# Performance work log

Hardware: AMD Instinct MI355X
Metric: run time of the kernel (lower is better)

Reference implementation:

```python
import jax, jax.numpy as jnp
import numpy as np

H, DH = 8, 32            # heads, per-head dim
F_DIM = H * DH           # hidden_channels = 256
N_P, N_A = 100000, 50000 # paper / author node counts
E_AP, E_PA, E_PP = 300000, 300000, 500000
N_CLASSES = 32


def _seg_softmax(alpha, idx, n):
    # softmax over edges grouped by destination node (per head)
    m = jax.ops.segment_max(alpha, idx, num_segments=n)
    m = jnp.where(jnp.isfinite(m), m, 0.0)  # nodes with no in-edges
    e = jnp.exp(alpha - m[idx])
    s = jax.ops.segment_sum(e, idx, num_segments=n)
    return e / (s[idx] + 1e-16)


def _edge_attn(h_src, h_dst, a_src, a_dst, src, dst, n_dst):
    # h_*: [N, H, DH]; a_*: [H, DH]; src/dst: [E]
    als = jnp.einsum('nhd,hd->nh', h_src, a_src)
    ald = jnp.einsum('nhd,hd->nh', h_dst, a_dst)
    alpha = jax.nn.leaky_relu(als[src] + ald[dst], negative_slope=0.2)  # [E,H]
    a = _seg_softmax(alpha, dst, n_dst)
    out = jax.ops.segment_sum(h_src[src] * a[:, :, None], dst, num_segments=n_dst)
    return jax.nn.relu(out).reshape(n_dst, F_DIM)


def _semantic(xs, kW, kb, q):
    # semantic (edge-type level) attention, PyG HANConv 'group'
    X = jnp.stack(xs)  # [K, N, F]
    score = jnp.einsum('f,kf->k', q, jnp.tanh(X @ kW + kb).mean(axis=1))
    attn = jax.nn.softmax(score)
    return jnp.einsum('k,knf->nf', attn, X)


def _han_layer(xP, xA, prm, edg):
    (W_P, b_P, W_A, b_A, aS_AP, aD_AP, aS_PA, aD_PA, aS_PP, aD_PP, kW, kb, q) = prm
    sAP, dAP, sPA, dPA, sPP, dPP = edg
    hP = (xP @ W_P + b_P).reshape(-1, H, DH)
    hA = (xA @ W_A + b_A).reshape(-1, H, DH)
    oAP = _edge_attn(hA, hP, aS_AP, aD_AP, sAP, dAP, N_P)  # author->paper
    oPP = _edge_attn(hP, hP, aS_PP, aD_PP, sPP, dPP, N_P)  # paper->paper
    oPA = _edge_attn(hP, hA, aS_PA, aD_PA, sPA, dPA, N_A)  # paper->author
    newP = _semantic([oAP, oPP], kW, kb, q)
    newA = _semantic([oPA], kW, kb, q)
    return newP, newA


def setup_inputs() -> dict:
    ks = iter(jax.random.split(jax.random.key(0), 80))
    def nrm(shape, scale=1.0):
        return jax.random.normal(next(ks), shape, dtype=jnp.float32) * scale
    def idx(n, high):
        return jax.random.randint(next(ks), (n,), 0, high, dtype=jnp.int32)
    inp = {}
    inp['x_P'] = nrm((N_P, 512))
    inp['x_A'] = nrm((N_A, 256))
    inp['src_AP'] = idx(E_AP, N_A); inp['dst_AP'] = idx(E_AP, N_P)
    inp['src_PA'] = idx(E_PA, N_P); inp['dst_PA'] = idx(E_PA, N_A)
    inp['src_PP'] = idx(E_PP, N_P); inp['dst_PP'] = idx(E_PP, N_P)
    for l, inP, inA in ((0, 512, 256), (1, F_DIM, F_DIM)):
        inp[f'W{l}_P'] = nrm((inP, F_DIM), 0.05)
        inp[f'b{l}_P'] = jnp.zeros((F_DIM,), jnp.float32)
        inp[f'W{l}_A'] = nrm((inA, F_DIM), 0.05)
        inp[f'b{l}_A'] = jnp.zeros((F_DIM,), jnp.float32)
        for et in ('AP', 'PA', 'PP'):
            inp[f'as{l}_{et}'] = nrm((H, DH), 0.1)
            inp[f'ad{l}_{et}'] = nrm((H, DH), 0.1)
        inp[f'k{l}_W'] = nrm((F_DIM, F_DIM), 0.05)
        inp[f'k{l}_b'] = jnp.zeros((F_DIM,), jnp.float32)
        inp[f'q{l}'] = nrm((F_DIM,), 0.1)
    inp['lin_W'] = nrm((F_DIM, N_CLASSES), 0.05)
    inp['lin_b'] = jnp.zeros((N_CLASSES,), jnp.float32)
    return inp


def reference(x_P, x_A, src_AP, dst_AP, src_PA, dst_PA, src_PP, dst_PP,
              W0_P, b0_P, W0_A, b0_A, as0_AP, ad0_AP, as0_PA, ad0_PA, as0_PP, ad0_PP, k0_W, k0_b, q0,
              W1_P, b1_P, W1_A, b1_A, as1_AP, ad1_AP, as1_PA, ad1_PA, as1_PP, ad1_PP, k1_W, k1_b, q1,
              lin_W, lin_b):
    edg = (src_AP, dst_AP, src_PA, dst_PA, src_PP, dst_PP)
    p0 = (W0_P, b0_P, W0_A, b0_A, as0_AP, ad0_AP, as0_PA, ad0_PA, as0_PP, ad0_PP, k0_W, k0_b, q0)
    p1 = (W1_P, b1_P, W1_A, b1_A, as1_AP, ad1_AP, as1_PA, ad1_PA, as1_PP, ad1_PP, k1_W, k1_b, q1)
    xP, xA = _han_layer(x_P, x_A, p0, edg)
    xP, xA = _han_layer(xP, xA, p1, edg)
    # final classifier on labeled_class = 'paper' (dropout is eval-mode no-op)
    return xP @ lin_W + lin_b
```

## Files before the change

kernel.cpp:

```cpp
#include <hip/hip_runtime.h>
#include <math.h>

typedef unsigned short u16;
typedef u16 ushort8 __attribute__((ext_vector_type(8)));
typedef __bf16 bf16x8 __attribute__((ext_vector_type(8)));
typedef float floatx4 __attribute__((ext_vector_type(4)));

__device__ __forceinline__ float bf2f(u16 u) {
  union { unsigned int i; float f; } v; v.i = ((unsigned int)u) << 16; return v.f;
}
__device__ __forceinline__ u16 f2bf(float f) {
  union { float f; unsigned int i; } v; v.f = f;
  return (u16)((v.i + 0x7fffu + ((v.i >> 16) & 1u)) >> 16);
}

#define CEILDIV(a, b) (((a) + (b) - 1) / (b))

typedef const __attribute__((address_space(1))) unsigned int ga_u32;
typedef __attribute__((address_space(3))) unsigned int lds_u32;
__device__ __forceinline__ void gload16(const u16* g, u16* l) {
  __builtin_amdgcn_global_load_lds((ga_u32*)g, (lds_u32*)l, 16, 0, 0);
}

__global__ void k_transpose(const float* __restrict__ W, u16* __restrict__ Wt, int K, int N) {
  int t = blockIdx.x * blockDim.x + threadIdx.x;
  if (t >= K * N) return;
  int n = t / K, k = t - n * K;
  Wt[t] = f2bf(W[k * N + n]);
}

__global__ void k_hist3(const int* __restrict__ d0, int E0, int* __restrict__ c0,
                        const int* __restrict__ d1, int E1, int* __restrict__ c1,
                        const int* __restrict__ d2, int E2, int* __restrict__ c2) {
  int t = blockIdx.x * blockDim.x + threadIdx.x;
  if (t < E0) atomicAdd(&c0[d0[t]], 1);
  else if (t < E0 + E1) atomicAdd(&c1[d1[t - E0]], 1);
  else if (t < E0 + E1 + E2) atomicAdd(&c2[d2[t - E0 - E1]], 1);
}

__global__ void k_scatter3(
    const int* __restrict__ d0, const int* __restrict__ s0v, int E0,
    const int* __restrict__ rp0, int* __restrict__ cur0, int* __restrict__ es0,
    const int* __restrict__ d1, const int* __restrict__ s1v, int E1,
    const int* __restrict__ rp1, int* __restrict__ cur1, int* __restrict__ es1,
    const int* __restrict__ d2, const int* __restrict__ s2v, int E2,
    const int* __restrict__ rp2, int* __restrict__ cur2, int* __restrict__ es2) {
  int t = blockIdx.x * blockDim.x + threadIdx.x;
  if (t < E0) {
    int d = d0[t];
    int p = atomicAdd(&cur0[d], 1);
    es0[rp0[d] + p] = s0v[t];
  } else if (t < E0 + E1) {
    int u = t - E0;
    int d = d1[u];
    int p = atomicAdd(&cur1[d], 1);
    es1[rp1[d] + p] = s1v[u];
  } else if (t < E0 + E1 + E2) {
    int u = t - E0 - E1;
    int d = d2[u];
    int p = atomicAdd(&cur2[d], 1);
    es2[rp2[d] + p] = s2v[u];
  }
}

__device__ __forceinline__ void seg_map(int b, int& seg, int& bs, int& n) {
  if (b < 98) { seg = 0; bs = b; n = 100000; }
  else if (b < 196) { seg = 1; bs = b - 98; n = 100000; }
  else { seg = 2; bs = b - 196; n = 50000; }
}

__global__ __launch_bounds__(256) void k_scan_a(
    const int* __restrict__ c0, const int* __restrict__ c1, const int* __restrict__ c2,
    int* __restrict__ bsum) {
  int seg, bs, n;
  seg_map(blockIdx.x, seg, bs, n);
  const int* cnt = seg == 0 ? c0 : (seg == 1 ? c1 : c2);
  int t = threadIdx.x;
  int base = bs * 1024 + t * 4;
  int s = 0;
#pragma unroll
  for (int j = 0; j < 4; j++) { int i = base + j; if (i < n) s += cnt[i]; }
#pragma unroll
  for (int o = 1; o < 64; o <<= 1) s += __shfl_xor(s, o);
  __shared__ int wt[4];
  int lane = t & 63, w = t >> 6;
  if (lane == 0) wt[w] = s;
  __syncthreads();
  if (t == 0) bsum[seg * 256 + bs] = wt[0] + wt[1] + wt[2] + wt[3];
}

__global__ __launch_bounds__(256) void k_scan_b(
    const int* __restrict__ bsum, int* __restrict__ bbase,
    int* __restrict__ rp0, int* __restrict__ rp1, int* __restrict__ rp2) {
  __shared__ int sm[256];
  int t = threadIdx.x;
  for (int seg = 0; seg < 3; ++seg) {
    int nb = (seg == 2) ? 49 : 98;
    int n = (seg == 2) ? 50000 : 100000;
    int v = (t < nb) ? bsum[seg * 256 + t] : 0;
    sm[t] = v;
    __syncthreads();
    for (int o = 1; o < 256; o <<= 1) {
      int u = (t >= o) ? sm[t - o] : 0;
      __syncthreads();
      sm[t] += u;
      __syncthreads();
    }
    if (t < nb) bbase[seg * 256 + t] = sm[t] - v;
    if (t == 255) {
      int* rp = seg == 0 ? rp0 : (seg == 1 ? rp1 : rp2);
      rp[n] = sm[255];
    }
    __syncthreads();
  }
}

__global__ __launch_bounds__(256) void k_scan_c(
    const int* __restrict__ c0, const int* __restrict__ c1, const int* __restrict__ c2,
    const int* __restrict__ bbase,
    int* __restrict__ rp0, int* __restrict__ rp1, int* __restrict__ rp2) {
  int seg, bs, n;
  seg_map(blockIdx.x, seg, bs, n);
  const int* cnt = seg == 0 ? c0 : (seg == 1 ? c1 : c2);
  int* rp = seg == 0 ? rp0 : (seg == 1 ? rp1 : rp2);
  int t = threadIdx.x;
  int base = bs * 1024 + t * 4;
  int c[4];
  int s = 0;
#pragma unroll
  for (int j = 0; j < 4; j++) { int i = base + j; c[j] = (i < n) ? cnt[i] : 0; s += c[j]; }
  int lane = t & 63, w = t >> 6;
  int incl = s;
#pragma unroll
  for (int o = 1; o < 64; o <<= 1) { int u = __shfl_up(incl, o); if (lane >= o) incl += u; }
  __shared__ int wt[4];
  if (lane == 63) wt[w] = incl;
  __syncthreads();
  int wb = 0;
#pragma unroll
  for (int j = 0; j < 4; j++) if (j < w) wb += wt[j];
  int thr = bbase[seg * 256 + bs] + wb + incl - s;
#pragma unroll
  for (int j = 0; j < 4; j++) { int i = base + j; if (i < n) rp[i] = thr; thr += c[j]; }
}

#define G3_BM 128
#define G3_BN 256
#define G3_BK 32

template <int SRC, int MODE>
__global__ __launch_bounds__(512, 4) void k_gemm3(
    const void* __restrict__ Av, const u16* __restrict__ A2, const float* __restrict__ attn,
    const u16* __restrict__ Bt, const float* __restrict__ bias,
    u16* __restrict__ Cb, float* __restrict__ colsum, int M, int K) {
  __shared__ __align__(16) u16 sm[2][(G3_BM + G3_BN) * G3_BK];
  int tid = threadIdx.x;
  int lane = tid & 63, wid = tid >> 6;
  int wm = wid >> 2, wn = wid & 3;
  int quad = lane >> 4, l16 = lane & 15;
  int m0 = blockIdx.x * G3_BM;

  float a0s = 0.f, a1s = 0.f;
  if (SRC == 1) { a0s = attn[0]; a1s = attn[1]; }

  int gr_ = tid >> 2;
  int gc_ = (tid & 3) * 8;
  int arow = m0 + gr_; if (arow >= M) arow = M - 1;
  const u16* gaB = (SRC != 2) ? (const u16*)Av + (size_t)arow * K + gc_ : nullptr;
  const u16* ga2 = (SRC == 1) ? A2 + (size_t)arow * K + gc_ : nullptr;
  const float* gaF = (SRC == 2) ? (const float*)Av + (size_t)arow * K + gc_ : nullptr;
  const u16* gb0 = Bt + (size_t)gr_ * K + gc_;
  const u16* gb1 = Bt + (size_t)(128 + gr_) * K + gc_;
  const int laA = wid * 512;
  const int laB0 = 4096 + wid * 512;
  const int laB1 = 8192 + wid * 512;

  floatx4 acc[4][4];
#pragma unroll
  for (int i = 0; i < 4; i++)
#pragma unroll
    for (int j = 0; j < 4; j++) acc[i][j] = (floatx4){0.f, 0.f, 0.f, 0.f};

  auto stage = [&](int buf, int k0) {
    u16* sa = sm[buf];
    if (SRC == 0) {
      gload16(gaB + k0, sa + laA);
    } else if (SRC == 2) {
      const floatx4* p = (const floatx4*)(gaF + k0);
      floatx4 v0 = p[0], v1 = p[1];
      u16 t[8];
#pragma unroll
      for (int j = 0; j < 4; j++) { t[j] = f2bf(v0[j]); t[4 + j] = f2bf(v1[j]); }
      *(ushort8*)(sa + laA + (lane << 3)) = *(ushort8*)t;
    } else {
      ushort8 u = *(const ushort8*)(gaB + k0);
      ushort8 w = *(const ushort8*)(ga2 + k0);
      u16 t[8];
#pragma unroll
      for (int j = 0; j < 8; j++) t[j] = f2bf(a0s * bf2f(u[j]) + a1s * bf2f(w[j]));
      *(ushort8*)(sa + laA + (lane << 3)) = *(ushort8*)t;
    }
    gload16(gb0 + k0, sa + laB0);
    gload16(gb1 + k0, sa + laB1);
  };

  stage(0, 0);
  __syncthreads();

  int nk = K / G3_BK;
  for (int t = 0; t < nk; ++t) {
    int cur = t & 1;
    if (t + 1 < nk) stage(cur ^ 1, (t + 1) * G3_BK);
    const u16* Ab = sm[cur];
    const u16* Bb = sm[cur] + G3_BM * G3_BK;
    bf16x8 af[4], bfr[4];
#pragma unroll
    for (int mi = 0; mi < 4; mi++)
      af[mi] = *(const bf16x8*)(Ab + (wm * 64 + mi * 16 + l16) * G3_BK + quad * 8);
#pragma unroll
    for (int ni = 0; ni < 4; ni++)
      bfr[ni] = *(const bf16x8*)(Bb + (wn * 64 + ni * 16 + l16) * G3_BK + quad * 8);
#pragma unroll
    for (int mi = 0; mi < 4; mi++)
#pragma unroll
      for (int ni = 0; ni < 4; ni++)
        acc[mi][ni] = __builtin_amdgcn_mfma_f32_16x16x32_bf16(af[mi], bfr[ni], acc[mi][ni], 0, 0, 0);
    __syncthreads();
  }

  if (MODE == 1) {
#pragma unroll
    for (int ni = 0; ni < 4; ni++) {
      int gc = wn * 64 + ni * 16 + l16;
      float bv = bias[gc];
      float part = 0.f;
#pragma unroll
      for (int mi = 0; mi < 4; mi++) {
#pragma unroll
        for (int r = 0; r < 4; r++) {
          int gr = m0 + wm * 64 + mi * 16 + quad * 4 + r;
          if (gr < M) {
            float v = acc[mi][ni][r] + bv;
            float e2 = __expf(2.f * v);
            part += 1.f - 2.f / (e2 + 1.f);
          }
        }
      }
      part += __shfl_xor(part, 16);
      part += __shfl_xor(part, 32);
      if (lane < 16) atomicAdd(&colsum[gc], part);
    }
  } else {
    float* smf = (float*)sm;
    float* tw = smf + wid * 16 * 68;
#pragma unroll
    for (int mi = 0; mi < 4; mi++) {
#pragma unroll
      for (int ni = 0; ni < 4; ni++)
#pragma unroll
        for (int r = 0; r < 4; r++)
          tw[(quad * 4 + r) * 68 + ni * 16 + l16] = acc[mi][ni][r];
      int row = lane >> 2, cq = (lane & 3) * 16;
      int gr = m0 + wm * 64 + mi * 16 + row;
      if (gr < M) {
        int gc0 = wn * 64 + cq;
        u16 ob[16];
#pragma unroll
        for (int j = 0; j < 16; j++) ob[j] = f2bf(tw[row * 68 + cq + j] + bias[gc0 + j]);
        *(ushort8*)(Cb + (size_t)gr * 256 + gc0) = *(ushort8*)ob;
        *(ushort8*)(Cb + (size_t)gr * 256 + gc0 + 8) = *(ushort8*)(ob + 8);
      }
    }
  }
}

#define BM 128
#define BN 128
#define BK 32

__global__ __launch_bounds__(256) void k_gemm2_cls(
    const u16* __restrict__ A, const u16* __restrict__ A2, const float* __restrict__ attn,
    const u16* __restrict__ Bt, const float* __restrict__ bias,
    float* __restrict__ Cf, int M, int N, int K) {
  __shared__ __align__(16) u16 sm[2][2][BM * BK];
  int tid = threadIdx.x;
  int lane = tid & 63, wid = tid >> 6;
  int wm = wid >> 1, wn = wid & 1;
  int quad = lane >> 4, l16 = lane & 15;
  int m0 = blockIdx.x * BM, n0 = 0;

  float a0s = attn[0], a1s = attn[1];

  int sr = lane >> 2;
  int sc = (lane & 3) * 8;
  int ra0 = m0 + wid * 32 + sr;
  int ra1 = ra0 + 16;
  int rb0 = n0 + wid * 32 + sr;
  int rb1 = rb0 + 16;
  if (ra0 >= M) ra0 = M - 1;
  if (ra1 >= M) ra1 = M - 1;
  if (rb0 >= N) rb0 = N - 1;
  if (rb1 >= N) rb1 = N - 1;
  const u16* ga0 = A + (size_t)ra0 * K + sc;
  const u16* ga1 = A + (size_t)ra1 * K + sc;
  const u16* g2a0 = A2 + (size_t)ra0 * K + sc;
  const u16* g2a1 = A2 + (size_t)ra1 * K + sc;
  const u16* gb0 = Bt + (size_t)rb0 * K + sc;
  const u16* gb1 = Bt + (size_t)rb1 * K + sc;
  const int la = wid * 32 * BK;
  const int lb = la + 16 * BK;

  floatx4 acc[4][4];
#pragma unroll
  for (int i = 0; i < 4; i++)
#pragma unroll
    for (int j = 0; j < 4; j++) acc[i][j] = (floatx4){0.f, 0.f, 0.f, 0.f};

  auto stage = [&](int buf, int k0) {
    u16* sa = &sm[buf][0][0];
    u16* sb = &sm[buf][1][0];
    ushort8 u0 = *(const ushort8*)(ga0 + k0);
    ushort8 w0 = *(const ushort8*)(g2a0 + k0);
    ushort8 u1 = *(const ushort8*)(ga1 + k0);
    ushort8 w1 = *(const ushort8*)(g2a1 + k0);
    u16 t0[8], t1[8];
#pragma unroll
    for (int j = 0; j < 8; j++) {
      t0[j] = f2bf(a0s * bf2f(u0[j]) + a1s * bf2f(w0[j]));
      t1[j] = f2bf(a0s * bf2f(u1[j]) + a1s * bf2f(w1[j]));
    }
    *(ushort8*)(sa + la + lane * 8) = *(ushort8*)t0;
    *(ushort8*)(sa + lb + lane * 8) = *(ushort8*)t1;
    gload16(gb0 + k0, sb + la);
    gload16(gb1 + k0, sb + lb);
  };

  stage(0, 0);
  __syncthreads();

  int nk = K / BK;
  for (int t = 0; t < nk; ++t) {
    int cur = t & 1;
    if (t + 1 < nk) stage(cur ^ 1, (t + 1) * BK);
    const u16* Ab = &sm[cur][0][0];
    const u16* Bb = &sm[cur][1][0];
    bf16x8 af[4], bfr[4];
#pragma unroll
    for (int mi = 0; mi < 4; mi++)
      af[mi] = *(const bf16x8*)(Ab + (wm * 64 + mi * 16 + l16) * BK + quad * 8);
#pragma unroll
    for (int ni = 0; ni < 4; ni++)
      bfr[ni] = *(const bf16x8*)(Bb + (wn * 64 + ni * 16 + l16) * BK + quad * 8);
#pragma unroll
    for (int mi = 0; mi < 4; mi++)
#pragma unroll
      for (int ni = 0; ni < 4; ni++)
        acc[mi][ni] = __builtin_amdgcn_mfma_f32_16x16x32_bf16(af[mi], bfr[ni], acc[mi][ni], 0, 0, 0);
    __syncthreads();
  }

#pragma unroll
  for (int ni = 0; ni < 4; ni++) {
    int gc = n0 + wn * 64 + ni * 16 + l16;
    if (gc >= N) continue;
    float bv = bias[gc];
#pragma unroll
    for (int mi = 0; mi < 4; mi++) {
#pragma unroll
      for (int r = 0; r < 4; r++) {
        int gr = m0 + wm * 64 + mi * 16 + quad * 4 + r;
        if (gr < M) Cf[(size_t)gr * N + gc] = acc[mi][ni][r] + bv;
      }
    }
  }
}

__global__ void k_logits(const u16* __restrict__ h, int N,
                         const float* __restrict__ a0, const float* __restrict__ a1,
                         const float* __restrict__ a2, const float* __restrict__ a3,
                         float* __restrict__ o0, float* __restrict__ o1,
                         float* __restrict__ o2, float* __restrict__ o3) {
  int t = blockIdx.x * blockDim.x + threadIdx.x;
  int n = t >> 3, hh = t & 7;
  if (n >= N) return;
  const ushort8* hp = (const ushort8*)(h + (size_t)n * 256 + hh * 32);
  float d0 = 0.f, d1 = 0.f, d2 = 0.f, d3 = 0.f;
#pragma unroll
  for (int q = 0; q < 4; q++) {
    ushort8 v = hp[q];
#pragma unroll
    for (int j = 0; j < 8; j++) {
      float f = bf2f(v[j]);
      int idx = hh * 32 + q * 8 + j;
      d0 += f * a0[idx];
      d1 += f * a1[idx];
      if (a2) d2 += f * a2[idx];
      if (a3) d3 += f * a3[idx];
    }
  }
  o0[t] = d0;
  o1[t] = d1;
  if (o2) o2[t] = d2;
  if (o3) o3[t] = d3;
}

__global__ __launch_bounds__(256) void k_attn_agg(
    const int* __restrict__ rp, const int* __restrict__ esrc,
    const float* __restrict__ als, const float* __restrict__ ald,
    const u16* __restrict__ hsrc, u16* __restrict__ out, int Ndst) {
  int wid = threadIdx.x >> 6, lane = threadIdx.x & 63;
  int n = blockIdx.x * 4 + wid;
  if (n >= Ndst) return;
  int hh = lane >> 3;
  int b = rp[n], e = rp[n + 1];
  float av = ald[n * 8 + hh];
  float m = -1e30f, s = 0.f;
  float a0 = 0.f, a1 = 0.f, a2 = 0.f, a3 = 0.f;
  int i = b;
  for (; i + 3 < e; i += 4) {
    int s0 = esrc[i], s1 = esrc[i + 1], s2 = esrc[i + 2], s3 = esrc[i + 3];
    float x0 = als[s0 * 8 + hh] + av, x1 = als[s1 * 8 + hh] + av;
    float x2 = als[s2 * 8 + hh] + av, x3 = als[s3 * 8 + hh] + av;
    ushort4 v0 = *(const ushort4*)(hsrc + (size_t)s0 * 256 + lane * 4);
    ushort4 v1 = *(const ushort4*)(hsrc + (size_t)s1 * 256 + lane * 4);
    ushort4 v2 = *(const ushort4*)(hsrc + (size_t)s2 * 256 + lane * 4);
    ushort4 v3 = *(const ushort4*)(hsrc + (size_t)s3 * 256 + lane * 4);
    x0 = x0 > 0.f ? x0 : 0.2f * x0;
    x1 = x1 > 0.f ? x1 : 0.2f * x1;
    x2 = x2 > 0.f ? x2 : 0.2f * x2;
    x3 = x3 > 0.f ? x3 : 0.2f * x3;
    float mx = fmaxf(fmaxf(x0, x1), fmaxf(x2, x3));
    if (mx > m) {
      float r = __expf(m - mx);
      s *= r; a0 *= r; a1 *= r; a2 *= r; a3 *= r;
      m = mx;
    }
    float w0 = __expf(x0 - m), w1 = __expf(x1 - m);
    float w2 = __expf(x2 - m), w3 = __expf(x3 - m);
    s += (w0 + w1) + (w2 + w3);
    a0 += w0 * bf2f(v0.x) + w1 * bf2f(v1.x) + w2 * bf2f(v2.x) + w3 * bf2f(v3.x);
    a1 += w0 * bf2f(v0.y) + w1 * bf2f(v1.y) + w2 * bf2f(v2.y) + w3 * bf2f(v3.y);
    a2 += w0 * bf2f(v0.z) + w1 * bf2f(v1.z) + w2 * bf2f(v2.z) + w3 * bf2f(v3.z);
    a3 += w0 * bf2f(v0.w) + w1 * bf2f(v1.w) + w2 * bf2f(v2.w) + w3 * bf2f(v3.w);
  }
  for (; i < e; ++i) {
    int s0 = esrc[i];
    float x0 = als[s0 * 8 + hh] + av;
    ushort4 v0 = *(const ushort4*)(hsrc + (size_t)s0 * 256 + lane * 4);
    x0 = x0 > 0.f ? x0 : 0.2f * x0;
    if (x0 > m) {
      float r = __expf(m - x0);
      s *= r; a0 *= r; a1 *= r; a2 *= r; a3 *= r;
      m = x0;
    }
    float w0 = __expf(x0 - m);
    s += w0;
    a0 += w0 * bf2f(v0.x);
    a1 += w0 * bf2f(v0.y);
    a2 += w0 * bf2f(v0.z);
    a3 += w0 * bf2f(v0.w);
  }
  float inv = 1.f / (s + 1e-16f);
  a0 *= inv; a1 *= inv; a2 *= inv; a3 *= inv;
  ushort4 o;
  o.x = f2bf(a0 > 0.f ? a0 : 0.f);
  o.y = f2bf(a1 > 0.f ? a1 : 0.f);
  o.z = f2bf(a2 > 0.f ? a2 : 0.f);
  o.w = f2bf(a3 > 0.f ? a3 : 0.f);
  *(ushort4*)(out + (size_t)n * 256 + lane * 4) = o;
}

__global__ void k_scores(const float* __restrict__ cs0, const float* __restrict__ cs1,
                         const float* __restrict__ q, float invN, float* __restrict__ attn) {
  int lane = threadIdx.x;
  float p0 = 0.f, p1 = 0.f;
  for (int f = lane; f < 256; f += 64) {
    float qv = q[f];
    p0 += qv * cs0[f];
    p1 += qv * cs1[f];
  }
  for (int o = 32; o > 0; o >>= 1) {
    p0 += __shfl_down(p0, o);
    p1 += __shfl_down(p1, o);
  }
  if (lane == 0) {
    float s0 = p0 * invN, s1 = p1 * invN;
    float mx = fmaxf(s0, s1);
    float e0 = __expf(s0 - mx), e1 = __expf(s1 - mx);
    float den = e0 + e1;
    attn[0] = e0 / den;
    attn[1] = e1 / den;
  }
}

extern "C" void kernel_launch(void* const* d_in, const int* in_sizes, int n_in,
                              void* d_out, int out_size, void* d_ws, size_t ws_size,
                              hipStream_t stream) {
  const int NP = 100000, NA = 50000;
  const int EAP = 300000, EPA = 300000, EPP = 500000;

  const float* xP = (const float*)d_in[0];
  const float* xA = (const float*)d_in[1];
  const int* srcAP = (const int*)d_in[2];
  const int* dstAP = (const int*)d_in[3];
  const int* srcPA = (const int*)d_in[4];
  const int* dstPA = (const int*)d_in[5];
  const int* srcPP = (const int*)d_in[6];
  const int* dstPP = (const int*)d_in[7];
  const float *W_P[2], *b_P[2], *W_A[2], *b_A[2];
  const float *asAP[2], *adAP[2], *asPA[2], *adPA[2], *asPP[2], *adPP[2];
  const float *kW[2], *kb[2], *qv[2];
  for (int l = 0; l < 2; ++l) {
    int base = 8 + l * 13;
    W_P[l] = (const float*)d_in[base + 0];
    b_P[l] = (const float*)d_in[base + 1];
    W_A[l] = (const float*)d_in[base + 2];
    b_A[l] = (const float*)d_in[base + 3];
    asAP[l] = (const float*)d_in[base + 4];
    adAP[l] = (const float*)d_in[base + 5];
    asPA[l] = (const float*)d_in[base + 6];
    adPA[l] = (const float*)d_in[base + 7];
    asPP[l] = (const float*)d_in[base + 8];
    adPP[l] = (const float*)d_in[base + 9];
    kW[l] = (const float*)d_in[base + 10];
    kb[l] = (const float*)d_in[base + 11];
    qv[l] = (const float*)d_in[base + 12];
  }
  const float* linW = (const float*)d_in[34];
  const float* linb = (const float*)d_in[35];

  char* ws = (char*)d_ws;
  size_t off = 0;
  auto alloc = [&](size_t bytes) -> char* {
    char* p = ws + off;
    off += (bytes + 255) & ~(size_t)255;
    return p;
  };
  u16* P1 = (u16*)alloc((size_t)NP * 256 * 2);
  u16* P2 = (u16*)alloc((size_t)NP * 256 * 2);
  u16* A1 = (u16*)alloc((size_t)NA * 256 * 2);
  u16* A2 = (u16*)alloc((size_t)NA * 256 * 2);
  u16* P3 = (u16*)alloc((size_t)NP * 256 * 2);
  float* ldAP_P = (float*)alloc((size_t)NP * 8 * 4);
  float* lsPA_P = (float*)alloc((size_t)NP * 8 * 4);
  float* lsPP_P = (float*)alloc((size_t)NP * 8 * 4);
  float* ldPP_P = (float*)alloc((size_t)NP * 8 * 4);
  float* lsAP_A = (float*)alloc((size_t)NA * 8 * 4);
  float* ldPA_A = (float*)alloc((size_t)NA * 8 * 4);
  u16* wtP0 = (u16*)alloc(256 * 512 * 2);
  u16* wtA0 = (u16*)alloc(256 * 256 * 2);
  u16* wtP1 = (u16*)alloc(256 * 256 * 2);
  u16* wtA1 = (u16*)alloc(256 * 256 * 2);
  u16* kwt0 = (u16*)alloc(256 * 256 * 2);
  u16* kwt1 = (u16*)alloc(256 * 256 * 2);
  u16* lwt = (u16*)alloc(32 * 256 * 2);
  int* rpAP = (int*)alloc((NP + 1) * 4);
  int* rpPP = (int*)alloc((NP + 1) * 4);
  int* rpPA = (int*)alloc((NA + 1) * 4);
  int* eiAP = (int*)alloc((size_t)EAP * 4);
  int* eiPP = (int*)alloc((size_t)EPP * 4);
  int* eiPA = (int*)alloc((size_t)EPA * 4);
  int* bsum = (int*)alloc(768 * 4);
  int* bbase = (int*)alloc(768 * 4);
  size_t zbytes = (size_t)(4 * NP + 2 * NA) * 4 + 4 * 256 * 4;
  char* zblock = alloc(zbytes);
  int* cntAP = (int*)zblock;
  int* cntPP = cntAP + NP;
  int* cntPA = cntPP + NP;
  int* curAP = cntPA + NA;
  int* curPP = curAP + NP;
  int* curPA = curPP + NP;
  float* cs = (float*)(curPA + NA);
  float* attnBuf = (float*)alloc(256);

  u16* HP = A1;
  u16* hA0 = P2;
  u16* P2b = P2 + (size_t)NA * 256;

  (void)hipMemsetAsync((void*)zblock, 0, zbytes, stream);

  k_transpose<<<CEILDIV(512 * 256, 256), 256, 0, stream>>>(W_P[0], wtP0, 512, 256);
  k_transpose<<<CEILDIV(256 * 256, 256), 256, 0, stream>>>(W_A[0], wtA0, 256, 256);
  k_transpose<<<CEILDIV(256 * 256, 256), 256, 0, stream>>>(W_P[1], wtP1, 256, 256);
  k_transpose<<<CEILDIV(256 * 256, 256), 256, 0, stream>>>(W_A[1], wtA1, 256, 256);
  k_transpose<<<CEILDIV(256 * 256, 256), 256, 0, stream>>>(kW[0], kwt0, 256, 256);
  k_transpose<<<CEILDIV(256 * 256, 256), 256, 0, stream>>>(kW[1], kwt1, 256, 256);
  k_transpose<<<CEILDIV(256 * 32, 256), 256, 0, stream>>>(linW, lwt, 256, 32);

  k_hist3<<<CEILDIV(EAP + EPP + EPA, 256), 256, 0, stream>>>(
      dstAP, EAP, cntAP, dstPP, EPP, cntPP, dstPA, EPA, cntPA);
  k_scan_a<<<245, 256, 0, stream>>>(cntAP, cntPP, cntPA, bsum);
  k_scan_b<<<1, 256, 0, stream>>>(bsum, bbase, rpAP, rpPP, rpPA);
  k_scan_c<<<245, 256, 0, stream>>>(cntAP, cntPP, cntPA, bbase, rpAP, rpPP, rpPA);
  k_scatter3<<<CEILDIV(EAP + EPP + EPA, 256), 256, 0, stream>>>(
      dstAP, srcAP, EAP, rpAP, curAP, eiAP,
      dstPP, srcPP, EPP, rpPP, curPP, eiPP,
      dstPA, srcPA, EPA, rpPA, curPA, eiPA);

  int gP = CEILDIV(NP, G3_BM), gA = CEILDIV(NA, G3_BM);

  k_gemm3<2, 0><<<gP, 512, 0, stream>>>(xP, nullptr, nullptr, wtP0, b_P[0], HP, nullptr, NP, 512);
  k_gemm3<2, 0><<<gA, 512, 0, stream>>>(xA, nullptr, nullptr, wtA0, b_A[0], hA0, nullptr, NA, 256);

  k_logits<<<CEILDIV(NP * 8, 256), 256, 0, stream>>>(
      HP, NP, adAP[0], asPA[0], asPP[0], adPP[0], ldAP_P, lsPA_P, lsPP_P, ldPP_P);
  k_logits<<<CEILDIV(NA * 8, 256), 256, 0, stream>>>(
      hA0, NA, asAP[0], adPA[0], nullptr, nullptr, lsAP_A, ldPA_A, nullptr, nullptr);
  k_attn_agg<<<CEILDIV(NP, 4), 256, 0, stream>>>(rpPP, eiPP, lsPP_P, ldPP_P, HP, P1, NP);
  k_attn_agg<<<CEILDIV(NA, 4), 256, 0, stream>>>(rpPA, eiPA, lsPA_P, ldPA_A, HP, P2b, NA);
  k_attn_agg<<<CEILDIV(NP, 4), 256, 0, stream>>>(rpAP, eiAP, lsAP_A, ldAP_P, hA0, HP, NP);
  k_gemm3<0, 1><<<gP, 512, 0, stream>>>(HP, nullptr, nullptr, kwt0, kb[0], nullptr, cs, NP, 256);
  k_gemm3<0, 1><<<gP, 512, 0, stream>>>(P1, nullptr, nullptr, kwt0, kb[0], nullptr, cs + 256, NP, 256);
  k_scores<<<1, 64, 0, stream>>>(cs, cs + 256, qv[0], 1.0f / NP, attnBuf);
  k_gemm3<1, 0><<<gP, 512, 0, stream>>>(HP, P1, attnBuf, wtP1, b_P[1], P3, nullptr, NP, 256);

  k_gemm3<0, 0><<<gA, 512, 0, stream>>>(P2b, nullptr, nullptr, wtA1, b_A[1], hA0, nullptr, NA, 256);
  k_logits<<<CEILDIV(NP * 8, 256), 256, 0, stream>>>(
      P3, NP, adAP[1], asPA[1], asPP[1], adPP[1], ldAP_P, lsPA_P, lsPP_P, ldPP_P);
  k_logits<<<CEILDIV(NA * 8, 256), 256, 0, stream>>>(
      hA0, NA, asAP[1], adPA[1], nullptr, nullptr, lsAP_A, ldPA_A, nullptr, nullptr);
  k_attn_agg<<<CEILDIV(NP, 4), 256, 0, stream>>>(rpPP, eiPP, lsPP_P, ldPP_P, P3, P1, NP);
  k_attn_agg<<<CEILDIV(NP, 4), 256, 0, stream>>>(rpAP, eiAP, lsAP_A, ldAP_P, hA0, HP, NP);
  k_gemm3<0, 1><<<gP, 512, 0, stream>>>(HP, nullptr, nullptr, kwt1, kb[1], nullptr, cs + 512, NP, 256);
  k_gemm3<0, 1><<<gP, 512, 0, stream>>>(P1, nullptr, nullptr, kwt1, kb[1], nullptr, cs + 768, NP, 256);
  k_scores<<<1, 64, 0, stream>>>(cs + 512, cs + 768, qv[1], 1.0f / NP, attnBuf + 2);

  k_gemm2_cls<<<CEILDIV(NP, BM), 256, 0, stream>>>(
      HP, P1, attnBuf + 2, lwt, linb, (float*)d_out, NP, 32, 256);
}
```

Measured before the change: 1.370 ms.

## Fuse attention logits into GEMM epilogue and batch small kernels into combined launches

Computes the per-head attention logits inside the projection GEMM epilogue, so the separate logits kernels no longer re-read the bf16 hidden features. The three (then two) edge-attention aggregation launches are merged into one multi-segment kernel, the paired colsum GEMMs become a single double-grid launch, and the seven weight transposes become one launch. Buffers are reassigned (P3/HP swapped) so the aggregated outputs do not overwrite inputs still needed. This cuts launch overhead and one full pass over the node features, at the cost of extra register pressure and FMA work in the GEMM epilogue, computed from fp32 values before bf16 rounding.

```diff
diff --git a/kernel.cpp b/kernel.cpp
--- a/kernel.cpp
+++ b/kernel.cpp
@@ -22,11 +22,26 @@
   __builtin_amdgcn_global_load_lds((ga_u32*)g, (lds_u32*)l, 16, 0, 0);
 }
 
-__global__ void k_transpose(const float* __restrict__ W, u16* __restrict__ Wt, int K, int N) {
+__global__ void k_transpose7(
+    const float* __restrict__ W0, u16* __restrict__ T0,
+    const float* __restrict__ W1, u16* __restrict__ T1,
+    const float* __restrict__ W2, u16* __restrict__ T2,
+    const float* __restrict__ W3, u16* __restrict__ T3,
+    const float* __restrict__ W4, u16* __restrict__ T4,
+    const float* __restrict__ W5, u16* __restrict__ T5,
+    const float* __restrict__ W6, u16* __restrict__ T6) {
   int t = blockIdx.x * blockDim.x + threadIdx.x;
-  if (t >= K * N) return;
-  int n = t / K, k = t - n * K;
-  Wt[t] = f2bf(W[k * N + n]);
+  const float* W; u16* T; int K, N, u;
+  if (t < 131072) { W = W0; T = T0; K = 512; N = 256; u = t; }
+  else if (t < 196608) { W = W1; T = T1; K = 256; N = 256; u = t - 131072; }
+  else if (t < 262144) { W = W2; T = T2; K = 256; N = 256; u = t - 196608; }
+  else if (t < 327680) { W = W3; T = T3; K = 256; N = 256; u = t - 262144; }
+  else if (t < 393216) { W = W4; T = T4; K = 256; N = 256; u = t - 327680; }
+  else if (t < 458752) { W = W5; T = T5; K = 256; N = 256; u = t - 393216; }
+  else if (t < 466944) { W = W6; T = T6; K = 256; N = 32; u = t - 458752; }
+  else return;
+  int n = u / K, k = u - n * K;
+  T[u] = f2bf(W[k * N + n]);
 }
 
 __global__ void k_hist3(const int* __restrict__ d0, int E0, int* __restrict__ c0,
@@ -148,17 +163,26 @@
 #define G3_BN 256
 #define G3_BK 32
 
-template <int SRC, int MODE>
+template <int SRC, int MODE, int NL, int PAIR>
 __global__ __launch_bounds__(512, 4) void k_gemm3(
     const void* __restrict__ Av, const u16* __restrict__ A2, const float* __restrict__ attn,
     const u16* __restrict__ Bt, const float* __restrict__ bias,
-    u16* __restrict__ Cb, float* __restrict__ colsum, int M, int K) {
+    u16* __restrict__ Cb, float* __restrict__ colsum, int M, int K,
+    const float* __restrict__ av0, const float* __restrict__ av1,
+    const float* __restrict__ av2, const float* __restrict__ av3,
+    float* __restrict__ lo0, float* __restrict__ lo1,
+    float* __restrict__ lo2, float* __restrict__ lo3) {
   __shared__ __align__(16) u16 sm[2][(G3_BM + G3_BN) * G3_BK];
+  int bid = blockIdx.x;
+  if (PAIR) {
+    int half = (int)gridDim.x >> 1;
+    if (bid >= half) { bid -= half; Av = (const void*)A2; colsum += 256; }
+  }
   int tid = threadIdx.x;
   int lane = tid & 63, wid = tid >> 6;
   int wm = wid >> 2, wn = wid & 3;
   int quad = lane >> 4, l16 = lane & 15;
-  int m0 = blockIdx.x * G3_BM;
+  int m0 = bid * G3_BM;
 
   float a0s = 0.f, a1s = 0.f;
   if (SRC == 1) { a0s = attn[0]; a1s = attn[1]; }
@@ -262,20 +286,40 @@
           tw[(quad * 4 + r) * 68 + ni * 16 + l16] = acc[mi][ni][r];
       int row = lane >> 2, cq = (lane & 3) * 16;
       int gr = m0 + wm * 64 + mi * 16 + row;
+      int gc0 = wn * 64 + cq;
+      u16 ob[16];
+      float p0 = 0.f, p1 = 0.f, p2 = 0.f, p3 = 0.f;
+#pragma unroll
+      for (int j = 0; j < 16; j++) {
+        float v = tw[row * 68 + cq + j] + bias[gc0 + j];
+        ob[j] = f2bf(v);
+        if (NL > 0) {
+          int col = gc0 + j;
+          p0 += v * av0[col];
+          p1 += v * av1[col];
+          if (NL > 2) { p2 += v * av2[col]; p3 += v * av3[col]; }
+        }
+      }
       if (gr < M) {
-        int gc0 = wn * 64 + cq;
-        u16 ob[16];
-#pragma unroll
-        for (int j = 0; j < 16; j++) ob[j] = f2bf(tw[row * 68 + cq + j] + bias[gc0 + j]);
         *(ushort8*)(Cb + (size_t)gr * 256 + gc0) = *(ushort8*)ob;
         *(ushort8*)(Cb + (size_t)gr * 256 + gc0 + 8) = *(ushort8*)(ob + 8);
       }
+      if (NL > 0) {
+        p0 += __shfl_xor(p0, 1);
+        p1 += __shfl_xor(p1, 1);
+        if (NL > 2) { p2 += __shfl_xor(p2, 1); p3 += __shfl_xor(p3, 1); }
+        if ((lane & 1) == 0 && gr < M) {
+          int hd = wn * 2 + ((lane & 3) >> 1);
+          lo0[gr * 8 + hd] = p0;
+          lo1[gr * 8 + hd] = p1;
+          if (NL > 2) { lo2[gr * 8 + hd] = p2; lo3[gr * 8 + hd] = p3; }
+        }
+      }
     }
   }
 }
 
 #define BM 128
-#define BN 128
 #define BK 32
 
 __global__ __launch_bounds__(256) void k_gemm2_cls(
@@ -375,41 +419,27 @@
   }
 }
 
-__global__ void k_logits(const u16* __restrict__ h, int N,
-                         const float* __restrict__ a0, const float* __restrict__ a1,
-                         const float* __restrict__ a2, const float* __restrict__ a3,
-                         float* __restrict__ o0, float* __restrict__ o1,
-                         float* __restrict__ o2, float* __restrict__ o3) {
-  int t = blockIdx.x * blockDim.x + threadIdx.x;
-  int n = t >> 3, hh = t & 7;
-  if (n >= N) return;
-  const ushort8* hp = (const ushort8*)(h + (size_t)n * 256 + hh * 32);
-  float d0 = 0.f, d1 = 0.f, d2 = 0.f, d3 = 0.f;
-#pragma unroll
-  for (int q = 0; q < 4; q++) {
-    ushort8 v = hp[q];
-#pragma unroll
-    for (int j = 0; j < 8; j++) {
-      float f = bf2f(v[j]);
-      int idx = hh * 32 + q * 8 + j;
-      d0 += f * a0[idx];
-      d1 += f * a1[idx];
-      if (a2) d2 += f * a2[idx];
-      if (a3) d3 += f * a3[idx];
-    }
-  }
-  o0[t] = d0;
-  o1[t] = d1;
-  if (o2) o2[t] = d2;
-  if (o3) o3[t] = d3;
-}
-
-__global__ __launch_bounds__(256) void k_attn_agg(
-    const int* __restrict__ rp, const int* __restrict__ esrc,
-    const float* __restrict__ als, const float* __restrict__ ald,
-    const u16* __restrict__ hsrc, u16* __restrict__ out, int Ndst) {
+__global__ __launch_bounds__(256) void k_attn3(
+    int nb0, int nb1,
+    const int* __restrict__ rp0, const int* __restrict__ es0, const float* __restrict__ als0,
+    const float* __restrict__ ald0, const u16* __restrict__ h0, u16* __restrict__ out0, int N0,
+    const int* __restrict__ rp1, const int* __restrict__ es1, const float* __restrict__ als1,
+    const float* __restrict__ ald1, const u16* __restrict__ h1, u16* __restrict__ out1, int N1,
+    const int* __restrict__ rp2, const int* __restrict__ es2, const float* __restrict__ als2,
+    const float* __restrict__ ald2, const u16* __restrict__ h2, u16* __restrict__ out2, int N2) {
+  int bid = blockIdx.x;
+  const int* rp; const int* esrc; const float* als; const float* ald;
+  const u16* hsrc; u16* out; int Ndst;
+  if (bid < nb0) { rp = rp0; esrc = es0; als = als0; ald = ald0; hsrc = h0; out = out0; Ndst = N0; }
+  else if (bid < nb0 + nb1) {
+    bid -= nb0;
+    rp = rp1; esrc = es1; als = als1; ald = ald1; hsrc = h1; out = out1; Ndst = N1;
+  } else {
+    bid -= nb0 + nb1;
+    rp = rp2; esrc = es2; als = als2; ald = ald2; hsrc = h2; out = out2; Ndst = N2;
+  }
   int wid = threadIdx.x >> 6, lane = threadIdx.x & 63;
-  int n = blockIdx.x * 4 + wid;
+  int n = bid * 4 + wid;
   if (n >= Ndst) return;
   int hh = lane >> 3;
   int b = rp[n], e = rp[n + 1];
@@ -579,13 +609,9 @@
 
   (void)hipMemsetAsync((void*)zblock, 0, zbytes, stream);
 
-  k_transpose<<<CEILDIV(512 * 256, 256), 256, 0, stream>>>(W_P[0], wtP0, 512, 256);
-  k_transpose<<<CEILDIV(256 * 256, 256), 256, 0, stream>>>(W_A[0], wtA0, 256, 256);
-  k_transpose<<<CEILDIV(256 * 256, 256), 256, 0, stream>>>(W_P[1], wtP1, 256, 256);
-  k_transpose<<<CEILDIV(256 * 256, 256), 256, 0, stream>>>(W_A[1], wtA1, 256, 256);
-  k_transpose<<<CEILDIV(256 * 256, 256), 256, 0, stream>>>(kW[0], kwt0, 256, 256);
-  k_transpose<<<CEILDIV(256 * 256, 256), 256, 0, stream>>>(kW[1], kwt1, 256, 256);
-  k_transpose<<<CEILDIV(256 * 32, 256), 256, 0, stream>>>(linW, lwt, 256, 32);
+  k_transpose7<<<CEILDIV(466944, 256), 256, 0, stream>>>(
+      W_P[0], wtP0, W_A[0], wtA0, W_P[1], wtP1, W_A[1], wtA1,
+      kW[0], kwt0, kW[1], kwt1, linW, lwt);
 
   k_hist3<<<CEILDIV(EAP + EPP + EPA, 256), 256, 0, stream>>>(
       dstAP, EAP, cntAP, dstPP, EPP, cntPP, dstPA, EPA, cntPA);
@@ -598,33 +624,45 @@
       dstPA, srcPA, EPA, rpPA, curPA, eiPA);
 
   int gP = CEILDIV(NP, G3_BM), gA = CEILDIV(NA, G3_BM);
-
-  k_gemm3<2, 0><<<gP, 512, 0, stream>>>(xP, nullptr, nullptr, wtP0, b_P[0], HP, nullptr, NP, 512);
-  k_gemm3<2, 0><<<gA, 512, 0, stream>>>(xA, nullptr, nullptr, wtA0, b_A[0], hA0, nullptr, NA, 256);
-
-  k_logits<<<CEILDIV(NP * 8, 256), 256, 0, stream>>>(
-      HP, NP, adAP[0], asPA[0], asPP[0], adPP[0], ldAP_P, lsPA_P, lsPP_P, ldPP_P);
-  k_logits<<<CEILDIV(NA * 8, 256), 256, 0, stream>>>(
-      hA0, NA, asAP[0], adPA[0], nullptr, nullptr, lsAP_A, ldPA_A, nullptr, nullptr);
-  k_attn_agg<<<CEILDIV(NP, 4), 256, 0, stream>>>(rpPP, eiPP, lsPP_P, ldPP_P, HP, P1, NP);
-  k_attn_agg<<<CEILDIV(NA, 4), 256, 0, stream>>>(rpPA, eiPA, lsPA_P, ldPA_A, HP, P2b, NA);
-  k_attn_agg<<<CEILDIV(NP, 4), 256, 0, stream>>>(rpAP, eiAP, lsAP_A, ldAP_P, hA0, HP, NP);
-  k_gemm3<0, 1><<<gP, 512, 0, stream>>>(HP, nullptr, nullptr, kwt0, kb[0], nullptr, cs, NP, 256);
-  k_gemm3<0, 1><<<gP, 512, 0, stream>>>(P1, nullptr, nullptr, kwt0, kb[0], nullptr, cs + 256, NP, 256);
+  int bP = CEILDIV(NP, 4), bA = CEILDIV(NA, 4);
+
+  k_gemm3<2, 0, 4, 0><<<gP, 512, 0, stream>>>(
+      xP, nullptr, nullptr, wtP0, b_P[0], HP, nullptr, NP, 512,
+      adAP[0], asPA[0], asPP[0], adPP[0], ldAP_P, lsPA_P, lsPP_P, ldPP_P);
+  k_gemm3<2, 0, 2, 0><<<gA, 512, 0, stream>>>(
+      xA, nullptr, nullptr, wtA0, b_A[0], hA0, nullptr, NA, 256,
+      asAP[0], adPA[0], nullptr, nullptr, lsAP_A, ldPA_A, nullptr, nullptr);
+
+  k_attn3<<<bP + bA + bP, 256, 0, stream>>>(
+      bP, bA,
+      rpPP, eiPP, lsPP_P, ldPP_P, HP, P1, NP,
+      rpPA, eiPA, lsPA_P, ldPA_A, HP, P2b, NA,
+      rpAP, eiAP, lsAP_A, ldAP_P, hA0, P3, NP);
+
+  k_gemm3<0, 1, 0, 1><<<2 * gP, 512, 0, stream>>>(
+      P3, P1, nullptr, kwt0, kb[0], nullptr, cs, NP, 256,
+      nullptr, nullptr, nullptr, nullptr, nullptr, nullptr, nullptr, nullptr);
   k_scores<<<1, 64, 0, stream>>>(cs, cs + 256, qv[0], 1.0f / NP, attnBuf);
-  k_gemm3<1, 0><<<gP, 512, 0, stream>>>(HP, P1, attnBuf, wtP1, b_P[1], P3, nullptr, NP, 256);
-
-  k_gemm3<0, 0><<<gA, 512, 0, stream>>>(P2b, nullptr, nullptr, wtA1, b_A[1], hA0, nullptr, NA, 256);
-  k_logits<<<CEILDIV(NP * 8, 256), 256, 0, stream>>>(
-      P3, NP, adAP[1], asPA[1], asPP[1], adPP[1], ldAP_P, lsPA_P, lsPP_P, ldPP_P);
-  k_logits<<<CEILDIV(NA * 8, 256), 256, 0, stream>>>(
-      hA0, NA, asAP[1], adPA[1], nullptr, nullptr, lsAP_A, ldPA_A, nullptr, nullptr);
-  k_attn_agg<<<CEILDIV(NP, 4), 256, 0, stream>>>(rpPP, eiPP, lsPP_P, ldPP_P, P3, P1, NP);
-  k_attn_agg<<<CEILDIV(NP, 4), 256, 0, stream>>>(rpAP, eiAP, lsAP_A, ldAP_P, hA0, HP, NP);
-  k_gemm3<0, 1><<<gP, 512, 0, stream>>>(HP, nullptr, nullptr, kwt1, kb[1], nullptr, cs + 512, NP, 256);
-  k_gemm3<0, 1><<<gP, 512, 0, stream>>>(P1, nullptr, nullptr, kwt1, kb[1], nullptr, cs + 768, NP, 256);
+
+  k_gemm3<1, 0, 4, 0><<<gP, 512, 0, stream>>>(
+      P3, P1, attnBuf, wtP1, b_P[1], HP, nullptr, NP, 256,
+      adAP[1], asPA[1], asPP[1], adPP[1], ldAP_P, lsPA_P, lsPP_P, ldPP_P);
+
+  k_gemm3<0, 0, 2, 0><<<gA, 512, 0, stream>>>(
+      P2b, nullptr, nullptr, wtA1, b_A[1], hA0, nullptr, NA, 256,
+      asAP[1], adPA[1], nullptr, nullptr, lsAP_A, ldPA_A, nullptr, nullptr);
+
+  k_attn3<<<bP + bP, 256, 0, stream>>>(
+      bP, bP,
+      rpPP, eiPP, lsPP_P, ldPP_P, HP, P1, NP,
+      rpAP, eiAP, lsAP_A, ldAP_P, hA0, P3, NP,
+      nullptr, nullptr, nullptr, nullptr, nullptr, nullptr, 0);
+
+  k_gemm3<0, 1, 0, 1><<<2 * gP, 512, 0, stream>>>(
+      P3, P1, nullptr, kwt1, kb[1], nullptr, cs + 512, NP, 256,
+      nullptr, nullptr, nullptr, nullptr, nullptr, nullptr, nullptr, nullptr);
   k_scores<<<1, 64, 0, stream>>>(cs + 512, cs + 768, qv[1], 1.0f / NP, attnBuf + 2);
 
   k_gemm2_cls<<<CEILDIV(NP, BM), 256, 0, stream>>>(
-      HP, P1, attnBuf + 2, lwt, linb, (float*)d_out, NP, 32, 256);
-}
+      P3, P1, attnBuf + 2, lwt, linb, (float*)d_out, NP, 32, 256);
+}
```

After: 1.149 ms. 1.19x faster.
